# Kernel optimization log

Measured on AMD Instinct MI355X. Metric: run time of the kernel, lower is better.

## Reference

```python
import jax, jax.numpy as jnp
import numpy as np

H = 8  # num_heads in nn.MultiheadAttention


def setup_inputs() -> dict:
    key = jax.random.key(0)
    ks = jax.random.split(key, 8)
    B, S, D, M = 32, 64, 512, 8192
    query = jax.random.normal(ks[0], (B, S, D), dtype=jnp.float32)
    memory = jax.random.normal(ks[1], (B, S, D), dtype=jnp.float32)
    memory_bank = jax.random.normal(ks[2], (M, D), dtype=jnp.float32)
    # nn.MultiheadAttention params: packed in_proj (3D, D) + bias, out_proj (D, D) + bias
    in_proj_w = jax.random.normal(ks[3], (3 * D, D), dtype=jnp.float32) / np.sqrt(D)
    in_proj_b = jnp.zeros((3 * D,), dtype=jnp.float32)
    out_proj_w = jax.random.normal(ks[4], (D, D), dtype=jnp.float32) / np.sqrt(D)
    out_proj_b = jnp.zeros((D,), dtype=jnp.float32)
    return {
        "query": query,
        "memory": memory,
        "memory_bank": memory_bank,
        "in_proj_w": in_proj_w,
        "in_proj_b": in_proj_b,
        "out_proj_w": out_proj_w,
        "out_proj_b": out_proj_b,
        "ptr": 17,
    }


def _retrieve(query, memory_bank, in_proj_w, in_proj_b, out_proj_w, out_proj_b):
    B, S, D = query.shape
    M = memory_bank.shape[0]
    hd = D // H
    Wq, Wk, Wv = in_proj_w[:D], in_proj_w[D:2 * D], in_proj_w[2 * D:]
    bq, bk, bv = in_proj_b[:D], in_proj_b[D:2 * D], in_proj_b[2 * D:]
    # key/value come from memory_bank expanded over batch -> identical per batch,
    # so project once: [M, D]
    q = (query @ Wq.T + bq).reshape(B, S, H, hd)
    k = (memory_bank @ Wk.T + bk).reshape(M, H, hd)
    v = (memory_bank @ Wv.T + bv).reshape(M, H, hd)
    scale = 1.0 / np.sqrt(hd).astype(np.float32)
    scores = jnp.einsum('bshd,mhd->bhsm', q * scale, k)  # [B,H,S,M]
    attn = jax.nn.softmax(scores, axis=-1)
    out = jnp.einsum('bhsm,mhd->bshd', attn, v).reshape(B, S, D)
    return out @ out_proj_w.T + out_proj_b


def _store(memory, memory_bank, ptr):
    M, D = memory_bank.shape
    flat = memory.reshape(-1, D)  # [N, D], N < M so indices are unique
    N = flat.shape[0]
    idx = (ptr + jnp.arange(N)) % M  # vectorized circular-buffer scatter
    new_bank = memory_bank.at[idx].set(flat)
    new_ptr = (ptr + N) % M
    return new_bank, new_ptr


def reference(query, memory, memory_bank, in_proj_w, in_proj_b, out_proj_w, out_proj_b, ptr):
    retrieved = _retrieve(query, memory_bank, in_proj_w, in_proj_b, out_proj_w, out_proj_b)
    new_bank, _ = _store(memory, memory_bank, ptr)
    return retrieved, new_bank
```

## Files before the change

kernel.cpp:

```cpp
#include <hip/hip_runtime.h>


#define Dm  512
#define Mb  8192
#define BSr 2048

#define QSCALE 0.18033688011112042f

typedef float f32x4 __attribute__((ext_vector_type(4)));
typedef short bf16x4 __attribute__((ext_vector_type(4)));
typedef short bf16x8 __attribute__((ext_vector_type(8)));
typedef unsigned short u16x4 __attribute__((ext_vector_type(4)));
typedef unsigned short u16x8 __attribute__((ext_vector_type(8)));
typedef unsigned u32x4 __attribute__((ext_vector_type(4)));

#define MFMA(a, b, c) __builtin_amdgcn_mfma_f32_16x16x32_bf16((a), (b), (c), 0, 0, 0)

#if __has_builtin(__builtin_amdgcn_exp2f)
#define EXP2F(x) __builtin_amdgcn_exp2f(x)
#else
#define EXP2F(x) __expf((x)*0.6931471805599453f)
#endif

__device__ __forceinline__ unsigned short f32_bf16(float f) {
  unsigned u = __builtin_bit_cast(unsigned, f);
  u += 0x7FFFu + ((u >> 16) & 1u);
  return (unsigned short)(u >> 16);
}
__device__ __forceinline__ float bf16_f32(unsigned short h) {
  unsigned u = ((unsigned)h) << 16;
  return __builtin_bit_cast(float, u);
}
__device__ __forceinline__ unsigned pack_bf16_trunc(float a, float b) {
  return (__builtin_bit_cast(unsigned, a) >> 16) |
         (__builtin_bit_cast(unsigned, b) & 0xFFFF0000u);
}

__device__ __forceinline__ void gload16(const unsigned short* g, unsigned short* l) {
  __builtin_amdgcn_global_load_lds(
      (const __attribute__((address_space(1))) void*)g,
      (__attribute__((address_space(3))) void*)l, 16, 0, 0);
}

__global__ __launch_bounds__(256) void convert_all(
    const float* __restrict__ q, const float* __restrict__ bank,
    const float* __restrict__ Win, const float* __restrict__ bin,
    const float* __restrict__ Wout, const float* __restrict__ bout,
    unsigned short* __restrict__ q_c, unsigned short* __restrict__ bank_c,
    unsigned short* __restrict__ Win_c, unsigned short* __restrict__ bin_c,
    unsigned short* __restrict__ Wout_c, unsigned short* __restrict__ bout_c) {
  const int e = (blockIdx.x * 256 + threadIdx.x) * 4;
  const float* src; unsigned short* dst; int off;
  if (e < 1048576)      { src = q;    dst = q_c;    off = e; }
  else if (e < 5242880) { src = bank; dst = bank_c; off = e - 1048576; }
  else if (e < 6029312) { src = Win;  dst = Win_c;  off = e - 5242880; }
  else if (e < 6030848) { src = bin;  dst = bin_c;  off = e - 6029312; }
  else if (e < 6292992) { src = Wout; dst = Wout_c; off = e - 6030848; }
  else                  { src = bout; dst = bout_c; off = e - 6292992; }
  f32x4 v = *(const f32x4*)(src + off);
  u16x4 o;
#pragma unroll
  for (int j = 0; j < 4; ++j) o[j] = f32_bf16(v[j]);
  *(u16x4*)(dst + off) = o;
}

__global__ __launch_bounds__(256) void proj_fused(
    const unsigned short* __restrict__ q_c,
    const unsigned short* __restrict__ bank_c,
    const unsigned short* __restrict__ Win_c,
    const unsigned short* __restrict__ bin_c,
    unsigned short* __restrict__ q_s,
    unsigned short* __restrict__ k_s,
    unsigned short* __restrict__ vT_s) {
  __shared__ __align__(16) unsigned short Kst[128 * 72];
  __shared__ __align__(16) unsigned short Vst[64 * 136];
  const int lane = threadIdx.x & 63;
  const int wv   = threadIdx.x >> 6;
  const int l15  = lane & 15;
  const int qd   = lane >> 4;
  const f32x4 z4 = {0.f, 0.f, 0.f, 0.f};

  if (blockIdx.x < 128) {
    const int mbase = (blockIdx.x >> 3) * 128 + wv * 32;
    const int nbase = (blockIdx.x & 7) * 64;
    f32x4 acc[2][4];
#pragma unroll
    for (int ti = 0; ti < 2; ++ti)
#pragma unroll
      for (int j = 0; j < 4; ++j) acc[ti][j] = z4;

    const unsigned short* a0p = q_c + (mbase + l15) * Dm + qd * 8;
    const unsigned short* a1p = a0p + 16 * Dm;
    const unsigned short* wp  = Win_c + (nbase + l15) * Dm + qd * 8;

#pragma unroll 4
    for (int k0 = 0; k0 < Dm; k0 += 32) {
      bf16x8 a0 = *(const bf16x8*)(a0p + k0);
      bf16x8 a1 = *(const bf16x8*)(a1p + k0);
#pragma unroll
      for (int j = 0; j < 4; ++j) {
        bf16x8 b = *(const bf16x8*)(wp + j * 16 * Dm + k0);
        acc[0][j] = MFMA(a0, b, acc[0][j]);
        acc[1][j] = MFMA(a1, b, acc[1][j]);
      }
    }
#pragma unroll
    for (int ti = 0; ti < 2; ++ti) {
#pragma unroll
      for (int j = 0; j < 4; ++j) {
        const int n = nbase + j * 16 + l15;
        const float bf = bf16_f32(bin_c[n]);
#pragma unroll
        for (int r = 0; r < 4; ++r) {
          const int m = mbase + ti * 16 + qd * 4 + r;
          const unsigned idx = ((unsigned)(m >> 6) * 8u + (unsigned)(n >> 6)) * 4096u +
                               (unsigned)(m & 63) * 64u + (unsigned)(n & 63);
          q_s[idx] = f32_bf16((acc[ti][j][r] + bf) * QSCALE);
        }
      }
    }
    return;
  }

  const int idx   = blockIdx.x - 128;
  const int h     = (idx >> 3) & 7;
  const int mbase = ((idx & 7) * 8 + (idx >> 6)) * 128;

  f32x4 kacc[2][4], vacc[2][4];
#pragma unroll
  for (int ti = 0; ti < 2; ++ti)
#pragma unroll
    for (int j = 0; j < 4; ++j) { kacc[ti][j] = z4; vacc[ti][j] = z4; }

  const unsigned short* a0p = bank_c + (mbase + wv * 32 + l15) * Dm + qd * 8;
  const unsigned short* a1p = a0p + 16 * Dm;
  const unsigned short* wkp = Win_c + (Dm + h * 64 + l15) * Dm + qd * 8;
  const unsigned short* wvp = Win_c + (2 * Dm + h * 64 + l15) * Dm + qd * 8;

#pragma unroll 2
  for (int k0 = 0; k0 < Dm; k0 += 32) {
    bf16x8 a0 = *(const bf16x8*)(a0p + k0);
    bf16x8 a1 = *(const bf16x8*)(a1p + k0);
#pragma unroll
    for (int j = 0; j < 4; ++j) {
      bf16x8 wk  = *(const bf16x8*)(wkp + j * 16 * Dm + k0);
      bf16x8 wvv = *(const bf16x8*)(wvp + j * 16 * Dm + k0);
      kacc[0][j] = MFMA(a0, wk, kacc[0][j]);
      kacc[1][j] = MFMA(a1, wk, kacc[1][j]);
      vacc[0][j] = MFMA(a0, wvv, vacc[0][j]);
      vacc[1][j] = MFMA(a1, wvv, vacc[1][j]);
    }
  }

#pragma unroll
  for (int ti = 0; ti < 2; ++ti) {
#pragma unroll
    for (int j = 0; j < 4; ++j) {
      const int d = j * 16 + l15;
      const float bk = bf16_f32(bin_c[Dm + h * 64 + d]);
      const float bv = bf16_f32(bin_c[2 * Dm + h * 64 + d]);
#pragma unroll
      for (int r = 0; r < 4; ++r) {
        const int m = wv * 32 + ti * 16 + qd * 4 + r;
        Kst[m * 72 + d]  = f32_bf16(kacc[ti][j][r] + bk);
        Vst[d * 136 + m] = f32_bf16(vacc[ti][j][r] + bv);
      }
    }
  }
  __syncthreads();

#pragma unroll
  for (int p = 0; p < 4; ++p) {
    const int m  = p * 32 + (threadIdx.x >> 3);
    const int c8 = threadIdx.x & 7;
    const int d  = c8 * 8;
    *(u16x8*)(k_s + h * (Mb * 64) + (mbase + m) * 64 + ((c8 ^ (m & 7)) * 8)) =
        *(const u16x8*)(Kst + m * 72 + d);
  }
#pragma unroll
  for (int p = 0; p < 4; ++p) {
    const int d    = p * 16 + (threadIdx.x >> 4);
    const int m16  = threadIdx.x & 15;
    const int base = (m16 >> 2) * 32;
    const int q4   = (m16 & 3) * 4;
    u16x4 lo = *(const u16x4*)(Vst + d * 136 + base + q4);
    u16x4 hi = *(const u16x4*)(Vst + d * 136 + base + 16 + q4);
    u16x8 o  = __builtin_shufflevector(lo, hi, 0, 1, 2, 3, 4, 5, 6, 7);
    *(u16x8*)(vT_s + (h * 64 + d) * Mb + mbase + ((m16 ^ (d & 7)) * 8)) = o;
  }
}

__global__ __launch_bounds__(256, 2) void attn_partial(
    const unsigned short* __restrict__ q_s,
    const unsigned short* __restrict__ k_s,
    const unsigned short* __restrict__ vT_s,
    unsigned short* __restrict__ O_part,
    float* __restrict__ l_part) {
  __shared__ __align__(16) unsigned short Kbuf[2][128 * 64];
  __shared__ __align__(16) unsigned short Vbuf[2][64 * 128];

  const int lane = threadIdx.x & 63;
  const int wv   = threadIdx.x >> 6;
  const int l15  = lane & 15;
  const int qd   = lane >> 4;
  const int h    = blockIdx.x & 7;
  const int g    = blockIdx.x >> 3;
  const int part = g & 3;
  const int b    = (g >> 2) * 2 + (wv >> 1);
  const int bh   = b * 8 + h;
  const int s0   = (wv & 1) * 32;

  const unsigned short* kp = k_s  + h * (Mb * 64);
  const unsigned short* vp = vT_s + h * (Mb * 64);
  const int m0p = part * 2048;

  bf16x8 bQ[2][2];
  {
    const unsigned short* qp = q_s + bh * 4096;
#pragma unroll
    for (int sj = 0; sj < 2; ++sj)
#pragma unroll
      for (int ks = 0; ks < 2; ++ks)
        bQ[sj][ks] = *(const bf16x8*)(qp + (s0 + sj * 16 + l15) * 64 + ks * 32 + qd * 8);
  }

  const f32x4 z4 = {0.f, 0.f, 0.f, 0.f};
  f32x4 oacc[2][4];
  float lsum[2] = {0.f, 0.f};
#pragma unroll
  for (int sj = 0; sj < 2; ++sj)
#pragma unroll
    for (int dt = 0; dt < 4; ++dt) oacc[sj][dt] = z4;

  const int swz = (l15 & 7) * 8;

  auto stage = [&](int buf, int m0) {
    const unsigned short* gk = kp + (m0 + wv * 32 + (lane >> 3)) * 64 + (lane & 7) * 8;
    unsigned short* lk = &Kbuf[buf][(wv * 32) * 64];
#pragma unroll
    for (int i = 0; i < 4; ++i) gload16(gk + i * 8 * 64, lk + i * 8 * 64);
    const unsigned short* gv = vp + (wv * 16 + (lane >> 4)) * Mb + m0 + (lane & 15) * 8;
    unsigned short* lv = &Vbuf[buf][(wv * 16) * 128];
#pragma unroll
    for (int i = 0; i < 4; ++i) gload16(gv + i * 4 * Mb, lv + i * 4 * 128);
  };

  auto compute = [&](int buf) {
    const unsigned short* Kb = Kbuf[buf];
    const unsigned short* Vb = Vbuf[buf];
#pragma unroll
    for (int c2 = 0; c2 < 2; ++c2) {
      f32x4 sfr[4][2];
#pragma unroll
      for (int kt = 0; kt < 4; ++kt)
#pragma unroll
        for (int sj = 0; sj < 2; ++sj) sfr[kt][sj] = z4;
#pragma unroll
      for (int kt = 0; kt < 4; ++kt) {
        const int row = c2 * 64 + kt * 16 + l15;
#pragma unroll
        for (int ks = 0; ks < 2; ++ks) {
          bf16x8 aK = *(const bf16x8*)(Kb + row * 64 + ((ks * 32 + qd * 8) ^ swz));
#pragma unroll
          for (int sj = 0; sj < 2; ++sj)
            sfr[kt][sj] = MFMA(aK, bQ[sj][ks], sfr[kt][sj]);
        }
      }
      bf16x8 aP[2][2];
#pragma unroll
      for (int sj = 0; sj < 2; ++sj) {
#pragma unroll
        for (int c = 0; c < 2; ++c) {
          const f32x4 lo = sfr[c * 2][sj];
          const f32x4 hi = sfr[c * 2 + 1][sj];
          float e0 = EXP2F(lo[0]), e1 = EXP2F(lo[1]);
          float e2 = EXP2F(lo[2]), e3 = EXP2F(lo[3]);
          float e4 = EXP2F(hi[0]), e5 = EXP2F(hi[1]);
          float e6 = EXP2F(hi[2]), e7 = EXP2F(hi[3]);
          lsum[sj] += ((e0 + e1) + (e2 + e3)) + ((e4 + e5) + (e6 + e7));
          u32x4 pk;
          pk[0] = pack_bf16_trunc(e0, e1);
          pk[1] = pack_bf16_trunc(e2, e3);
          pk[2] = pack_bf16_trunc(e4, e5);
          pk[3] = pack_bf16_trunc(e6, e7);
          aP[sj][c] = __builtin_bit_cast(bf16x8, pk);
        }
      }
#pragma unroll
      for (int c = 0; c < 2; ++c) {
#pragma unroll
        for (int dt = 0; dt < 4; ++dt) {
          const int d = dt * 16 + l15;
          bf16x8 bV = *(const bf16x8*)(Vb + d * 128 + ((c2 * 64 + c * 32 + qd * 8) ^ swz));
#pragma unroll
          for (int sj = 0; sj < 2; ++sj)
            oacc[sj][dt] = MFMA(aP[sj][c], bV, oacc[sj][dt]);
        }
      }
    }
  };

  stage(0, m0p);
  __asm__ volatile("s_waitcnt vmcnt(0)" ::: "memory");
  __syncthreads();
#pragma unroll 1
  for (int t = 0; t < 15; ++t) {
    stage((t + 1) & 1, m0p + (t + 1) * 128);
    compute(t & 1);
    __asm__ volatile("s_waitcnt vmcnt(0)" ::: "memory");
    __syncthreads();
  }
  compute(1);

#pragma unroll
  for (int sj = 0; sj < 2; ++sj) {
    float v = lsum[sj];
    v += __shfl_xor(v, 16);
    v += __shfl_xor(v, 32);
    if (qd == 0) l_part[(bh * 4 + part) * 64 + s0 + sj * 16 + l15] = v;
  }

  unsigned short* Ob = O_part + (bh * 4 + part) * 4096;
#pragma unroll
  for (int sj = 0; sj < 2; ++sj)
#pragma unroll
    for (int dt = 0; dt < 4; ++dt)
#pragma unroll
      for (int r = 0; r < 4; ++r)
        Ob[(s0 + sj * 16 + qd * 4 + r) * 64 + dt * 16 + l15] = f32_bf16(oacc[sj][dt][r]);
}

__global__ __launch_bounds__(256) void combine_bank(
    const unsigned short* __restrict__ O_part, const float* __restrict__ l_part,
    unsigned short* __restrict__ a_stage,
    const float* __restrict__ memory, const float* __restrict__ bank,
    const int* __restrict__ ptrp, float* __restrict__ out_bank) {
  if (blockIdx.x < 1024) {
    const int e  = (blockIdx.x * 256 + threadIdx.x) * 4;
    const int bh = e >> 12;
    const int rem = e & 4095;
    const int s  = rem >> 6;
    const int d  = rem & 63;
    float acc[4] = {0.f, 0.f, 0.f, 0.f};
    float l = 0.f;
#pragma unroll
    for (int p = 0; p < 4; ++p) {
      u16x4 v = *(const u16x4*)(O_part + (bh * 4 + p) * 4096 + rem);
#pragma unroll
      for (int j = 0; j < 4; ++j) acc[j] += bf16_f32(v[j]);
      l += l_part[(bh * 4 + p) * 64 + s];
    }
    const int b = bh >> 3, h = bh & 7;
    u16x4 o;
#pragma unroll
    for (int j = 0; j < 4; ++j) o[j] = f32_bf16(acc[j] / l);
    *(u16x4*)(a_stage + (b * 64 + s) * 512 + h * 64 + d) = o;
  } else {
    const int t  = (blockIdx.x - 1024) * 256 + threadIdx.x;
    const int r  = t >> 7;
    const int c4 = (t & 127) * 4;
    const int ptr = ptrp[0];
    const unsigned off = (unsigned)(r - ptr + Mb) & (Mb - 1);
    const float* src = (off < (unsigned)BSr) ? memory + off * Dm + c4
                                             : bank + r * Dm + c4;
    *(f32x4*)(out_bank + r * Dm + c4) = *(const f32x4*)src;
  }
}

__global__ __launch_bounds__(256) void out_proj(
    const unsigned short* __restrict__ A,
    const unsigned short* __restrict__ W,
    const unsigned short* __restrict__ bias,
    float* __restrict__ out) {
  const int lane = threadIdx.x & 63;
  const int wv   = threadIdx.x >> 6;
  const int l15  = lane & 15;
  const int qd   = lane >> 4;
  const int mbase = blockIdx.y * 128 + wv * 32;
  const int nbase = blockIdx.x * 64;

  const f32x4 z4 = {0.f, 0.f, 0.f, 0.f};
  f32x4 acc[2][4];
#pragma unroll
  for (int ti = 0; ti < 2; ++ti)
#pragma unroll
    for (int j = 0; j < 4; ++j) acc[ti][j] = z4;

  const unsigned short* a0p = A + (mbase + l15) * Dm + qd * 8;
  const unsigned short* a1p = a0p + 16 * Dm;
  const unsigned short* wp  = W + (nbase + l15) * Dm + qd * 8;

#pragma unroll 4
  for (int k0 = 0; k0 < Dm; k0 += 32) {
    bf16x8 a0 = *(const bf16x8*)(a0p + k0);
    bf16x8 a1 = *(const bf16x8*)(a1p + k0);
#pragma unroll
    for (int j = 0; j < 4; ++j) {
      bf16x8 bfr = *(const bf16x8*)(wp + j * 16 * Dm + k0);
      acc[0][j] = MFMA(a0, bfr, acc[0][j]);
      acc[1][j] = MFMA(a1, bfr, acc[1][j]);
    }
  }

#pragma unroll
  for (int ti = 0; ti < 2; ++ti) {
#pragma unroll
    for (int j = 0; j < 4; ++j) {
      const int n = nbase + j * 16 + l15;
      const float bf = bf16_f32(bias[n]);
#pragma unroll
      for (int r = 0; r < 4; ++r) {
        const int m = mbase + ti * 16 + qd * 4 + r;
        out[m * Dm + n] = acc[ti][j][r] + bf;
      }
    }
  }
}

extern "C" void kernel_launch(void* const* d_in, const int* in_sizes, int n_in,
                              void* d_out, int out_size, void* d_ws, size_t ws_size,
                              hipStream_t stream) {
  const float* query = (const float*)d_in[0];
  const float* memry = (const float*)d_in[1];
  const float* bank  = (const float*)d_in[2];
  const float* Win   = (const float*)d_in[3];
  const float* bin   = (const float*)d_in[4];
  const float* Wout  = (const float*)d_in[5];
  const float* bout  = (const float*)d_in[6];
  const int*   ptrp  = (const int*)d_in[7];
  float* outf = (float*)d_out;

  char* ws = (char*)d_ws;
  unsigned short* q_c     = (unsigned short*)(ws);
  unsigned short* a_stage = (unsigned short*)(ws);
  unsigned short* bank_c  = (unsigned short*)(ws + (2u << 20));
  unsigned short* O_part  = (unsigned short*)(ws + (2u << 20));
  unsigned short* Win_c   = (unsigned short*)(ws + (10u << 20));
  unsigned short* Wout_c  = (unsigned short*)(ws + 12058624u);
  unsigned short* q_s     = (unsigned short*)(ws + (12u << 20));
  float*          l_part  = (float*)(ws + (14u << 20));
  unsigned short* bin_c   = (unsigned short*)(ws + 14942208u);
  unsigned short* bout_c  = (unsigned short*)(ws + 14945280u);

  unsigned short* kv = (unsigned short*)(outf + 1048576);
  unsigned short* k_s  = kv;
  unsigned short* vT_s = kv + 4194304;

  convert_all<<<6146, 256, 0, stream>>>(query, bank, Win, bin, Wout, bout,
                                        q_c, bank_c, Win_c, bin_c, Wout_c, bout_c);

  proj_fused<<<640, 256, 0, stream>>>(q_c, bank_c, Win_c, bin_c, q_s, k_s, vT_s);

  attn_partial<<<512, 256, 0, stream>>>(q_s, k_s, vT_s, O_part, l_part);

  combine_bank<<<5120, 256, 0, stream>>>(O_part, l_part, a_stage,
                                         memry, bank, ptrp, outf + 1048576);

  out_proj<<<dim3(8, 16), 256, 0, stream>>>(a_stage, Wout_c, bout_c, outf);
}
```

Baseline: 197.6 us.

## Stage projection GEMM tiles through swizzled LDS with double-buffered async loads

The projection kernel previously read A and weight fragments straight from global memory per wave. It now stages 128x64 tiles of inputs and weights into XOR-swizzled shared memory with global_load_lds, double-buffers them across the K loop, and gives each wave a 64x64 subtile. To match the swizzled tile layout, the convert kernel writes q, bank and Win in a swizzled column order. The query-projection tile grows to 128x128, cutting the grid from 640 to 576 blocks, and occupancy is set to 2 blocks per CU. This is meant to cut redundant global traffic and latency, at the cost of larger register use and LDS pressure.

```diff
diff --git a/kernel.cpp b/kernel.cpp
--- a/kernel.cpp
+++ b/kernel.cpp
@@ -50,21 +50,26 @@
     unsigned short* __restrict__ Win_c, unsigned short* __restrict__ bin_c,
     unsigned short* __restrict__ Wout_c, unsigned short* __restrict__ bout_c) {
   const int e = (blockIdx.x * 256 + threadIdx.x) * 4;
-  const float* src; unsigned short* dst; int off;
-  if (e < 1048576)      { src = q;    dst = q_c;    off = e; }
-  else if (e < 5242880) { src = bank; dst = bank_c; off = e - 1048576; }
-  else if (e < 6029312) { src = Win;  dst = Win_c;  off = e - 5242880; }
-  else if (e < 6030848) { src = bin;  dst = bin_c;  off = e - 6029312; }
-  else if (e < 6292992) { src = Wout; dst = Wout_c; off = e - 6030848; }
-  else                  { src = bout; dst = bout_c; off = e - 6292992; }
+  const float* src; unsigned short* dst; int off; int sw;
+  if (e < 1048576)      { src = q;    dst = q_c;    off = e;           sw = 1; }
+  else if (e < 5242880) { src = bank; dst = bank_c; off = e - 1048576; sw = 1; }
+  else if (e < 6029312) { src = Win;  dst = Win_c;  off = e - 5242880; sw = 1; }
+  else if (e < 6030848) { src = bin;  dst = bin_c;  off = e - 6029312; sw = 0; }
+  else if (e < 6292992) { src = Wout; dst = Wout_c; off = e - 6030848; sw = 0; }
+  else                  { src = bout; dst = bout_c; off = e - 6292992; sw = 0; }
   f32x4 v = *(const f32x4*)(src + off);
   u16x4 o;
 #pragma unroll
   for (int j = 0; j < 4; ++j) o[j] = f32_bf16(v[j]);
-  *(u16x4*)(dst + off) = o;
-}
-
-__global__ __launch_bounds__(256) void proj_fused(
+  int doff = off;
+  if (sw) {
+    const int row = off >> 9, col = off & 511;
+    doff = (off & ~511) | ((((col >> 3) ^ (row & 7)) << 3) | (col & 7));
+  }
+  *(u16x4*)(dst + doff) = o;
+}
+
+__global__ __launch_bounds__(256, 2) void proj_fused(
     const unsigned short* __restrict__ q_c,
     const unsigned short* __restrict__ bank_c,
     const unsigned short* __restrict__ Win_c,
@@ -72,121 +77,160 @@
     unsigned short* __restrict__ q_s,
     unsigned short* __restrict__ k_s,
     unsigned short* __restrict__ vT_s) {
-  __shared__ __align__(16) unsigned short Kst[128 * 72];
-  __shared__ __align__(16) unsigned short Vst[64 * 136];
+  __shared__ __align__(16) unsigned short sh[32768];
   const int lane = threadIdx.x & 63;
   const int wv   = threadIdx.x >> 6;
   const int l15  = lane & 15;
   const int qd   = lane >> 4;
+  const int mh   = wv & 1;
+  const int nh   = wv >> 1;
+
+  const unsigned short *Ag, *B0, *B1;
+  int h = 0, mbase, nbase = 0;
+  const bool iskv = blockIdx.x < 512;
+  if (iskv) {
+    const int idx = blockIdx.x;
+    h     = (idx >> 3) & 7;
+    mbase = ((idx & 7) * 8 + (idx >> 6)) * 128;
+    Ag = bank_c + mbase * Dm;
+    B0 = Win_c + (Dm + h * 64) * Dm;
+    B1 = Win_c + (2 * Dm + h * 64) * Dm;
+  } else {
+    const int idx = blockIdx.x - 512;
+    mbase = (idx >> 2) * 128;
+    nbase = (idx & 3) * 128;
+    Ag = q_c + mbase * Dm;
+    B0 = Win_c + nbase * Dm;
+    B1 = Win_c + (nbase + 64) * Dm;
+  }
+
+  auto Ab = [&](int buf) { return sh + buf * 8192; };
+  auto Bb = [&](int buf) { return sh + 16384 + buf * 8192; };
+
+  auto stage = [&](int buf, int t) {
+#pragma unroll
+    for (int i = 0; i < 4; ++i) {
+      const int chunk = i * 256 + wv * 64 + lane;
+      const int row = chunk >> 3, c8 = chunk & 7;
+      gload16(Ag + row * Dm + (t * 8 + c8) * 8,
+              Ab(buf) + (i * 256 + wv * 64) * 8);
+    }
+#pragma unroll
+    for (int i = 0; i < 4; ++i) {
+      const int chunk = i * 256 + wv * 64 + lane;
+      const int row = chunk >> 3, c8 = chunk & 7;
+      const unsigned short* wb = (row < 64) ? B0 + row * Dm : B1 + (row - 64) * Dm;
+      gload16(wb + (t * 8 + c8) * 8,
+              Bb(buf) + (i * 256 + wv * 64) * 8);
+    }
+  };
+
   const f32x4 z4 = {0.f, 0.f, 0.f, 0.f};
-
-  if (blockIdx.x < 128) {
-    const int mbase = (blockIdx.x >> 3) * 128 + wv * 32;
-    const int nbase = (blockIdx.x & 7) * 64;
-    f32x4 acc[2][4];
-#pragma unroll
-    for (int ti = 0; ti < 2; ++ti)
-#pragma unroll
-      for (int j = 0; j < 4; ++j) acc[ti][j] = z4;
-
-    const unsigned short* a0p = q_c + (mbase + l15) * Dm + qd * 8;
-    const unsigned short* a1p = a0p + 16 * Dm;
-    const unsigned short* wp  = Win_c + (nbase + l15) * Dm + qd * 8;
-
-#pragma unroll 4
-    for (int k0 = 0; k0 < Dm; k0 += 32) {
-      bf16x8 a0 = *(const bf16x8*)(a0p + k0);
-      bf16x8 a1 = *(const bf16x8*)(a1p + k0);
-#pragma unroll
-      for (int j = 0; j < 4; ++j) {
-        bf16x8 b = *(const bf16x8*)(wp + j * 16 * Dm + k0);
-        acc[0][j] = MFMA(a0, b, acc[0][j]);
-        acc[1][j] = MFMA(a1, b, acc[1][j]);
-      }
-    }
-#pragma unroll
-    for (int ti = 0; ti < 2; ++ti) {
-#pragma unroll
-      for (int j = 0; j < 4; ++j) {
-        const int n = nbase + j * 16 + l15;
-        const float bf = bf16_f32(bin_c[n]);
+  f32x4 acc[4][4];
+#pragma unroll
+  for (int mt = 0; mt < 4; ++mt)
+#pragma unroll
+    for (int nt = 0; nt < 4; ++nt) acc[mt][nt] = z4;
+
+  auto compute = [&](int buf) {
+#pragma unroll
+    for (int ks = 0; ks < 2; ++ks) {
+      bf16x8 af[4], bfr[4];
+#pragma unroll
+      for (int mt = 0; mt < 4; ++mt) {
+        const int row = mh * 64 + mt * 16 + l15;
+        af[mt] = *(const bf16x8*)(Ab(buf) + row * 64 + (((ks * 4 + qd) ^ (row & 7)) * 8));
+      }
+#pragma unroll
+      for (int nt = 0; nt < 4; ++nt) {
+        const int row = nh * 64 + nt * 16 + l15;
+        bfr[nt] = *(const bf16x8*)(Bb(buf) + row * 64 + (((ks * 4 + qd) ^ (row & 7)) * 8));
+      }
+#pragma unroll
+      for (int mt = 0; mt < 4; ++mt)
+#pragma unroll
+        for (int nt = 0; nt < 4; ++nt)
+          acc[mt][nt] = MFMA(af[mt], bfr[nt], acc[mt][nt]);
+    }
+  };
+
+  stage(0, 0);
+  __asm__ volatile("s_waitcnt vmcnt(0)" ::: "memory");
+  __syncthreads();
+#pragma unroll 1
+  for (int t = 0; t < 7; ++t) {
+    stage((t + 1) & 1, t + 1);
+    compute(t & 1);
+    __asm__ volatile("s_waitcnt vmcnt(0)" ::: "memory");
+    __syncthreads();
+  }
+  compute(1);
+  __syncthreads();
+
+  if (iskv) {
+    unsigned short* Kst = sh;
+    unsigned short* Vst = sh + 16384;
+    if (nh == 0) {
+#pragma unroll
+      for (int nt = 0; nt < 4; ++nt) {
+        const int d = nt * 16 + l15;
+        const float bk = bf16_f32(bin_c[Dm + h * 64 + d]);
+#pragma unroll
+        for (int mt = 0; mt < 4; ++mt)
+#pragma unroll
+          for (int r = 0; r < 4; ++r) {
+            const int m = mh * 64 + mt * 16 + qd * 4 + r;
+            Kst[m * 72 + d] = f32_bf16(acc[mt][nt][r] + bk);
+          }
+      }
+    } else {
+#pragma unroll
+      for (int nt = 0; nt < 4; ++nt) {
+        const int d = nt * 16 + l15;
+        const float bv = bf16_f32(bin_c[2 * Dm + h * 64 + d]);
+#pragma unroll
+        for (int mt = 0; mt < 4; ++mt)
+#pragma unroll
+          for (int r = 0; r < 4; ++r) {
+            const int m = mh * 64 + mt * 16 + qd * 4 + r;
+            Vst[d * 136 + m] = f32_bf16(acc[mt][nt][r] + bv);
+          }
+      }
+    }
+    __syncthreads();
+#pragma unroll
+    for (int p = 0; p < 4; ++p) {
+      const int m  = p * 32 + (threadIdx.x >> 3);
+      const int c8 = threadIdx.x & 7;
+      *(u16x8*)(k_s + h * (Mb * 64) + (mbase + m) * 64 + ((c8 ^ (m & 7)) * 8)) =
+          *(const u16x8*)(Kst + m * 72 + c8 * 8);
+    }
+#pragma unroll
+    for (int p = 0; p < 4; ++p) {
+      const int d    = p * 16 + (threadIdx.x >> 4);
+      const int m16  = threadIdx.x & 15;
+      const int base = (m16 >> 2) * 32;
+      const int q4   = (m16 & 3) * 4;
+      u16x4 lo = *(const u16x4*)(Vst + d * 136 + base + q4);
+      u16x4 hi = *(const u16x4*)(Vst + d * 136 + base + 16 + q4);
+      u16x8 o  = __builtin_shufflevector(lo, hi, 0, 1, 2, 3, 4, 5, 6, 7);
+      *(u16x8*)(vT_s + (h * 64 + d) * Mb + mbase + ((m16 ^ (d & 7)) * 8)) = o;
+    }
+  } else {
+#pragma unroll
+    for (int nt = 0; nt < 4; ++nt) {
+      const int n = nbase + nh * 64 + nt * 16 + l15;
+      const float bf = bf16_f32(bin_c[n]);
+#pragma unroll
+      for (int mt = 0; mt < 4; ++mt)
 #pragma unroll
         for (int r = 0; r < 4; ++r) {
-          const int m = mbase + ti * 16 + qd * 4 + r;
+          const int m = mbase + mh * 64 + mt * 16 + qd * 4 + r;
           const unsigned idx = ((unsigned)(m >> 6) * 8u + (unsigned)(n >> 6)) * 4096u +
                                (unsigned)(m & 63) * 64u + (unsigned)(n & 63);
-          q_s[idx] = f32_bf16((acc[ti][j][r] + bf) * QSCALE);
+          q_s[idx] = f32_bf16((acc[mt][nt][r] + bf) * QSCALE);
         }
-      }
-    }
-    return;
-  }
-
-  const int idx   = blockIdx.x - 128;
-  const int h     = (idx >> 3) & 7;
-  const int mbase = ((idx & 7) * 8 + (idx >> 6)) * 128;
-
-  f32x4 kacc[2][4], vacc[2][4];
-#pragma unroll
-  for (int ti = 0; ti < 2; ++ti)
-#pragma unroll
-    for (int j = 0; j < 4; ++j) { kacc[ti][j] = z4; vacc[ti][j] = z4; }
-
-  const unsigned short* a0p = bank_c + (mbase + wv * 32 + l15) * Dm + qd * 8;
-  const unsigned short* a1p = a0p + 16 * Dm;
-  const unsigned short* wkp = Win_c + (Dm + h * 64 + l15) * Dm + qd * 8;
-  const unsigned short* wvp = Win_c + (2 * Dm + h * 64 + l15) * Dm + qd * 8;
-
-#pragma unroll 2
-  for (int k0 = 0; k0 < Dm; k0 += 32) {
-    bf16x8 a0 = *(const bf16x8*)(a0p + k0);
-    bf16x8 a1 = *(const bf16x8*)(a1p + k0);
-#pragma unroll
-    for (int j = 0; j < 4; ++j) {
-      bf16x8 wk  = *(const bf16x8*)(wkp + j * 16 * Dm + k0);
-      bf16x8 wvv = *(const bf16x8*)(wvp + j * 16 * Dm + k0);
-      kacc[0][j] = MFMA(a0, wk, kacc[0][j]);
-      kacc[1][j] = MFMA(a1, wk, kacc[1][j]);
-      vacc[0][j] = MFMA(a0, wvv, vacc[0][j]);
-      vacc[1][j] = MFMA(a1, wvv, vacc[1][j]);
-    }
-  }
-
-#pragma unroll
-  for (int ti = 0; ti < 2; ++ti) {
-#pragma unroll
-    for (int j = 0; j < 4; ++j) {
-      const int d = j * 16 + l15;
-      const float bk = bf16_f32(bin_c[Dm + h * 64 + d]);
-      const float bv = bf16_f32(bin_c[2 * Dm + h * 64 + d]);
-#pragma unroll
-      for (int r = 0; r < 4; ++r) {
-        const int m = wv * 32 + ti * 16 + qd * 4 + r;
-        Kst[m * 72 + d]  = f32_bf16(kacc[ti][j][r] + bk);
-        Vst[d * 136 + m] = f32_bf16(vacc[ti][j][r] + bv);
-      }
-    }
-  }
-  __syncthreads();
-
-#pragma unroll
-  for (int p = 0; p < 4; ++p) {
-    const int m  = p * 32 + (threadIdx.x >> 3);
-    const int c8 = threadIdx.x & 7;
-    const int d  = c8 * 8;
-    *(u16x8*)(k_s + h * (Mb * 64) + (mbase + m) * 64 + ((c8 ^ (m & 7)) * 8)) =
-        *(const u16x8*)(Kst + m * 72 + d);
-  }
-#pragma unroll
-  for (int p = 0; p < 4; ++p) {
-    const int d    = p * 16 + (threadIdx.x >> 4);
-    const int m16  = threadIdx.x & 15;
-    const int base = (m16 >> 2) * 32;
-    const int q4   = (m16 & 3) * 4;
-    u16x4 lo = *(const u16x4*)(Vst + d * 136 + base + q4);
-    u16x4 hi = *(const u16x4*)(Vst + d * 136 + base + 16 + q4);
-    u16x8 o  = __builtin_shufflevector(lo, hi, 0, 1, 2, 3, 4, 5, 6, 7);
-    *(u16x8*)(vT_s + (h * 64 + d) * Mb + mbase + ((m16 ^ (d & 7)) * 8)) = o;
+    }
   }
 }
 
@@ -449,7 +493,7 @@
   convert_all<<<6146, 256, 0, stream>>>(query, bank, Win, bin, Wout, bout,
                                         q_c, bank_c, Win_c, bin_c, Wout_c, bout_c);
 
-  proj_fused<<<640, 256, 0, stream>>>(q_c, bank_c, Win_c, bin_c, q_s, k_s, vT_s);
+  proj_fused<<<576, 256, 0, stream>>>(q_c, bank_c, Win_c, bin_c, q_s, k_s, vT_s);
 
   attn_partial<<<512, 256, 0, stream>>>(q_s, k_s, vT_s, O_part, l_part);
 
```

Measured after the change: 167.7 us. 15.1% less time.
